# Performance work log

Hardware: AMD Instinct MI355X
Metric: run time of the kernel (lower is better)

The kernel has to match this reference:

```python
import jax, jax.numpy as jnp
import numpy as np

D_MODEL = 1024
D_STATE = 16
D_CONV = 4
EXPAND = 2
HEADDIM = 8
D_INNER = EXPAND * D_MODEL            # 2048
NHEADS = D_INNER // HEADDIM           # 256
CONV_DIM = D_INNER + 2 * D_STATE      # 2080 (ngroups=1)
D_IN_PROJ = 2 * D_INNER + 2 * D_STATE + NHEADS  # 4384
B_SZ, SEQ = 4, 2048
EPS = 1e-5


def setup_inputs() -> dict:
    key = jax.random.key(0)
    ks = jax.random.split(key, 8)
    return {
        "x": jax.random.normal(ks[0], (B_SZ, SEQ, D_MODEL), jnp.float32),
        "ln_w": jnp.ones((D_MODEL,), jnp.float32),
        "ln_b": jnp.zeros((D_MODEL,), jnp.float32),
        "W_in": jax.random.normal(ks[1], (D_MODEL, D_IN_PROJ), jnp.float32) * 0.02,
        "conv_w": jax.random.normal(ks[2], (D_CONV, 1, CONV_DIM), jnp.float32) * 0.2,
        "conv_b": jnp.zeros((CONV_DIM,), jnp.float32),
        "A_log": jnp.log(jax.random.uniform(ks[3], (NHEADS,), jnp.float32, 1.0, 16.0)),
        "Dp": jnp.ones((NHEADS,), jnp.float32) + 0.1 * jax.random.normal(ks[4], (NHEADS,), jnp.float32),
        "dt_bias": 0.5 * jax.random.normal(ks[5], (NHEADS,), jnp.float32),
        "rms_w": jnp.ones((D_INNER,), jnp.float32),
        "W_out": jax.random.normal(ks[6], (D_INNER, D_MODEL), jnp.float32) * 0.02,
    }


def _mamba_block(x, ln_w, ln_b, W_in, conv_w, conv_b, A_log, Dp, dt_bias, rms_w, W_out):
    B, L, _ = x.shape
    # pre-norm LayerNorm
    mu = jnp.mean(x, axis=-1, keepdims=True)
    var = jnp.mean((x - mu) ** 2, axis=-1, keepdims=True)
    xn = (x - mu) * jax.lax.rsqrt(var + EPS) * ln_w + ln_b

    # in_proj -> z, xBC, dt
    u = xn @ W_in                                    # (B, L, 4384)
    z = u[..., :D_INNER]
    xBC = u[..., D_INNER:D_INNER + CONV_DIM]
    dt = jax.nn.softplus(u[..., -NHEADS:] + dt_bias)  # (B, L, NHEADS)

    # causal depthwise conv1d + SiLU
    xp = jnp.pad(xBC, ((0, 0), (D_CONV - 1, 0), (0, 0)))
    xBC = jax.lax.conv_general_dilated(
        xp, conv_w, window_strides=(1,), padding="VALID",
        dimension_numbers=("NWC", "WIO", "NWC"), feature_group_count=CONV_DIM)
    xBC = jax.nn.silu(xBC + conv_b)

    xs = xBC[..., :D_INNER].reshape(B, L, NHEADS, HEADDIM)   # SSM input
    Bm = xBC[..., D_INNER:D_INNER + D_STATE]                  # (B, L, N)
    Cm = xBC[..., D_INNER + D_STATE:]                          # (B, L, N)

    A = -jnp.exp(A_log)                                       # (NHEADS,)

    def step(h, inp):
        # h: (B, H, P, N)
        x_t, B_t, C_t, dt_t = inp
        dA = jnp.exp(dt_t * A)                                 # (B, H)
        h = h * dA[..., None, None] + jnp.einsum("bh,bhp,bn->bhpn", dt_t, x_t, B_t)
        y = jnp.einsum("bhpn,bn->bhp", h, C_t)
        return h, y

    h0 = jnp.zeros((B, NHEADS, HEADDIM, D_STATE), x.dtype)
    _, ys = jax.lax.scan(step, h0, (xs.swapaxes(0, 1), Bm.swapaxes(0, 1),
                                     Cm.swapaxes(0, 1), dt.swapaxes(0, 1)))
    y = ys.swapaxes(0, 1) + Dp[None, None, :, None] * xs       # (B, L, H, P)
    y = y.reshape(B, L, D_INNER)

    # gated RMSNorm: rmsnorm(y * silu(z)) * weight
    g = y * jax.nn.silu(z)
    g = g * jax.lax.rsqrt(jnp.mean(g * g, axis=-1, keepdims=True) + EPS) * rms_w

    return x + g @ W_out


def reference(x, ln_w, ln_b, W_in, conv_w, conv_b, A_log, Dp, dt_bias, rms_w, W_out):
    return _mamba_block(x, ln_w, ln_b, W_in, conv_w, conv_b, A_log, Dp, dt_bias, rms_w, W_out)
```

## Files before the change

kernel.cpp:

```cpp
#include <hip/hip_runtime.h>

typedef __bf16 bf16;
typedef __attribute__((ext_vector_type(8))) __bf16 bf16x8;
typedef __attribute__((ext_vector_type(4))) float f32x4;

#define B_SZ 4
#define SEQ 2048
#define DM 1024
#define DIN 2048
#define NH 256
#define DSTATE 16
#define CONVD 2080
#define DPROJ 4384
#define NPAD1 4608
#define MROWS 8192
#define NC 64
#define LC 32
#define UROWB 8768

__device__ __forceinline__ void gload_lds16(const void* g, void* l) {
  __builtin_amdgcn_global_load_lds(
      (__attribute__((address_space(1))) void*)g,
      (__attribute__((address_space(3))) void*)l, 16, 0, 0);
}

template <int N>
__device__ __forceinline__ void vm_wait() {
  asm volatile("s_waitcnt vmcnt(%0)" ::"n"(N) : "memory");
}
__device__ __forceinline__ void bar() { asm volatile("s_barrier" ::: "memory"); }

__global__ void transpose_cvt(const float* __restrict__ W, bf16* __restrict__ WT,
                              int K, int N, int Npad) {
  __shared__ float tile[32][33];
  int k0 = blockIdx.x * 32, n0 = blockIdx.y * 32;
  int tx = threadIdx.x, ty = threadIdx.y;
#pragma unroll
  for (int j = 0; j < 4; j++) {
    int k = k0 + ty + 8 * j, n = n0 + tx;
    tile[ty + 8 * j][tx] = (k < K && n < N) ? W[(size_t)k * N + n] : 0.f;
  }
  __syncthreads();
#pragma unroll
  for (int j = 0; j < 4; j++) {
    int n = n0 + ty + 8 * j, k = k0 + tx;
    if (n < Npad && k < K) WT[(size_t)n * K + k] = (bf16)tile[tx][ty + 8 * j];
  }
}

__global__ __launch_bounds__(256) void ln_kernel(const float* __restrict__ x,
                                                 const float* __restrict__ lw,
                                                 const float* __restrict__ lb,
                                                 bf16* __restrict__ xn) {
  int row = blockIdx.x;
  int t = threadIdx.x;
  f32x4 v4 = ((const f32x4*)(x + (size_t)row * DM))[t];
  float v0 = v4[0], v1 = v4[1], v2 = v4[2], v3 = v4[3];
  float s = v0 + v1 + v2 + v3;
  float s2 = v0 * v0 + v1 * v1 + v2 * v2 + v3 * v3;
#pragma unroll
  for (int off = 32; off > 0; off >>= 1) {
    s += __shfl_down(s, off);
    s2 += __shfl_down(s2, off);
  }
  __shared__ float ps[8];
  int wave = t >> 6, lane = t & 63;
  if (lane == 0) { ps[wave] = s; ps[4 + wave] = s2; }
  __syncthreads();
  s = ps[0] + ps[1] + ps[2] + ps[3];
  s2 = ps[4] + ps[5] + ps[6] + ps[7];
  float mean = s * (1.f / DM);
  float var = s2 * (1.f / DM) - mean * mean;
  float rstd = rsqrtf(var + 1e-5f);
  f32x4 wv = ((const f32x4*)lw)[t];
  f32x4 bv = ((const f32x4*)lb)[t];
  bf16 o[4];
  o[0] = (bf16)((v0 - mean) * rstd * wv[0] + bv[0]);
  o[1] = (bf16)((v1 - mean) * rstd * wv[1] + bv[1]);
  o[2] = (bf16)((v2 - mean) * rstd * wv[2] + bv[2]);
  o[3] = (bf16)((v3 - mean) * rstd * wv[3] + bv[3]);
  bf16* dst = xn + (size_t)row * DM + t * 4;
  dst[0] = o[0]; dst[1] = o[1]; dst[2] = o[2]; dst[3] = o[3];
}

#define PHASE(MQ, NQ, P, STAGE_STMT)                                                       \
  {                                                                                        \
    const char* sa_ = lds + ((P) * 2 + MQ) * 16384;                                        \
    const char* sb_ = lds + 65536 + ((P) * 2 + NQ) * 16384;                                \
    bf16x8 a_[4][2], b_[2][2];                                                             \
    _Pragma("unroll") for (int mi = 0; mi < 4; mi++) {                                     \
      int lrow = wm * 64 + mi * 16 + lr16;                                                 \
      a_[mi][0] = *(const bf16x8*)(sa_ + lrow * 128 + ts0 * 16);                           \
      a_[mi][1] = *(const bf16x8*)(sa_ + lrow * 128 + ts1 * 16);                           \
    }                                                                                      \
    _Pragma("unroll") for (int ni = 0; ni < 2; ni++) {                                     \
      int lrow = wn * 32 + ni * 16 + lr16;                                                 \
      b_[ni][0] = *(const bf16x8*)(sb_ + lrow * 128 + ts0 * 16);                           \
      b_[ni][1] = *(const bf16x8*)(sb_ + lrow * 128 + ts1 * 16);                           \
    }                                                                                      \
    STAGE_STMT;                                                                            \
    __builtin_amdgcn_s_setprio(1);                                                         \
    _Pragma("unroll") for (int mi = 0; mi < 4; mi++)                                       \
      _Pragma("unroll") for (int ni = 0; ni < 2; ni++) {                                   \
        acc[MQ * 4 + mi][NQ * 2 + ni] = __builtin_amdgcn_mfma_f32_16x16x32_bf16(           \
            a_[mi][0], b_[ni][0], acc[MQ * 4 + mi][NQ * 2 + ni], 0, 0, 0);                 \
        acc[MQ * 4 + mi][NQ * 2 + ni] = __builtin_amdgcn_mfma_f32_16x16x32_bf16(           \
            a_[mi][1], b_[ni][1], acc[MQ * 4 + mi][NQ * 2 + ni], 0, 0, 0);                 \
      }                                                                                    \
    __builtin_amdgcn_s_setprio(0);                                                         \
  }

__global__ __launch_bounds__(512, 2) void gemm1_8p(const bf16* __restrict__ A,
                                                   const bf16* __restrict__ BT,
                                                   bf16* __restrict__ C) {
  __shared__ char lds[131072];
  int bid = blockIdx.x;
  int swz = (bid & 7) * 72 + (bid >> 3);
  int bm = swz / 18, bn = swz - (swz / 18) * 18;
  int m0 = bm * 256, n0 = bn * 256;
  int t = threadIdx.x, lane = t & 63, wave = t >> 6;
  int wm = wave >> 2, wn = wave & 3;
  int lr16 = lane & 15, kq = lane >> 4;
  int ts0 = kq ^ (lr16 & 7);
  int ts1 = (4 + kq) ^ (lr16 & 7);
  int sw = (lane & 7) ^ ((lane >> 3) & 7);
  int l8 = lane >> 3;
  int c0 = 2 * wave, c1 = 2 * wave + 1;
  int lr0 = c0 * 8 + l8, lr1 = c1 * 8 + l8;
  const char* Ab = (const char*)A;
  const char* Bb = (const char*)BT;
  int grA0 = m0 + (lr0 >> 6) * 128 + (lr0 & 63);
  int grA1 = m0 + (lr1 >> 6) * 128 + (lr1 & 63);
  int gcB0 = n0 + (lr0 >> 5) * 64 + (lr0 & 31);
  int gcB1 = n0 + (lr1 >> 5) * 64 + (lr1 & 31);

  auto stA = [&](int kt, int p, int mq) {
    char* slot = lds + (p * 2 + mq) * 16384;
    size_t ko = (size_t)kt * 128 + sw * 16;
    gload_lds16(Ab + (size_t)(grA0 + mq * 64) * 2048 + ko, slot + c0 * 1024);
    gload_lds16(Ab + (size_t)(grA1 + mq * 64) * 2048 + ko, slot + c1 * 1024);
  };
  auto stB = [&](int kt, int p, int nq) {
    char* slot = lds + 65536 + (p * 2 + nq) * 16384;
    size_t ko = (size_t)kt * 128 + sw * 16;
    gload_lds16(Bb + (size_t)(gcB0 + nq * 32) * 2048 + ko, slot + c0 * 1024);
    gload_lds16(Bb + (size_t)(gcB1 + nq * 32) * 2048 + ko, slot + c1 * 1024);
  };

  f32x4 acc[8][4] = {};
  stA(0, 0, 0); stB(0, 0, 0); stA(0, 0, 1); stB(0, 0, 1); stA(1, 1, 0); stB(1, 1, 0);
#pragma unroll 1
  for (int kt = 0; kt < 16; kt++) {
    int p = kt & 1;
    if (kt < 15) vm_wait<8>(); else vm_wait<4>();
    bar();
    PHASE(0, 0, p, { if (kt + 1 < 16) stA(kt + 1, p ^ 1, 1); });
    if (kt < 15) vm_wait<6>(); else vm_wait<0>();
    bar();
    PHASE(0, 1, p, { if (kt + 1 < 16) stB(kt + 1, p ^ 1, 1); });
    bar();
    PHASE(1, 0, p, { if (kt + 2 < 16) stA(kt + 2, p, 0); });
    bar();
    PHASE(1, 1, p, { if (kt + 2 < 16) stB(kt + 2, p, 0); });
  }
#pragma unroll
  for (int mq = 0; mq < 2; mq++)
#pragma unroll
    for (int mi = 0; mi < 4; mi++)
#pragma unroll
      for (int nq = 0; nq < 2; nq++)
#pragma unroll
        for (int ni = 0; ni < 2; ni++) {
          int row = m0 + wm * 128 + mq * 64 + mi * 16 + kq * 4;
          int col = n0 + wn * 64 + nq * 32 + ni * 16 + lr16;
          f32x4 v = acc[mq * 4 + mi][nq * 2 + ni];
          if (col < 4384) {
#pragma unroll
            for (int r = 0; r < 4; r++)
              C[(size_t)(row + r) * DPROJ + col] = (bf16)v[r];
          }
        }
}

__global__ __launch_bounds__(256) void gemm2_kernel(const bf16* __restrict__ A,
                                                    const bf16* __restrict__ BT,
                                                    int K, int ldc,
                                                    float* __restrict__ C,
                                                    const float* __restrict__ Xres) {
  __shared__ bf16 As[128 * 32];
  __shared__ bf16 Bs[128 * 32];
  int m0 = blockIdx.y * 128, n0 = blockIdx.x * 128;
  int t = threadIdx.x;
  int lane = t & 63, wave = t >> 6;
  int wm = wave >> 1, wn = wave & 1;
  int lr = lane & 15, kq = lane >> 4;
  f32x4 acc[4][4] = {};
  const char* Ab = (const char*)A;
  const char* Bb = (const char*)BT;
  size_t strideA = (size_t)K * 2;
  int r0 = t >> 2;
  int kb0 = (t & 3) * 16;
  int nk = K / 32;
  for (int kt = 0; kt < nk; ++kt) {
    size_t koff = (size_t)kt * 64;
    gload_lds16(Ab + (size_t)(m0 + r0) * strideA + koff + kb0, (char*)As + wave * 1024);
    gload_lds16(Ab + (size_t)(m0 + 64 + r0) * strideA + koff + kb0, (char*)As + 4096 + wave * 1024);
    gload_lds16(Bb + (size_t)(n0 + r0) * strideA + koff + kb0, (char*)Bs + wave * 1024);
    gload_lds16(Bb + (size_t)(n0 + 64 + r0) * strideA + koff + kb0, (char*)Bs + 4096 + wave * 1024);
    __syncthreads();
    bf16x8 af[4], bfr[4];
#pragma unroll
    for (int i = 0; i < 4; i++) af[i] = *(const bf16x8*)&As[(wm * 64 + i * 16 + lr) * 32 + kq * 8];
#pragma unroll
    for (int j = 0; j < 4; j++) bfr[j] = *(const bf16x8*)&Bs[(wn * 64 + j * 16 + lr) * 32 + kq * 8];
#pragma unroll
    for (int i = 0; i < 4; i++)
#pragma unroll
      for (int j = 0; j < 4; j++)
        acc[i][j] = __builtin_amdgcn_mfma_f32_16x16x32_bf16(af[i], bfr[j], acc[i][j], 0, 0, 0);
    __syncthreads();
  }
#pragma unroll
  for (int i = 0; i < 4; i++) {
    int row = m0 + wm * 64 + i * 16 + kq * 4;
#pragma unroll
    for (int j = 0; j < 4; j++) {
      int col = n0 + wn * 64 + j * 16 + lr;
#pragma unroll
      for (int r = 0; r < 4; r++) {
        size_t o = (size_t)(row + r) * ldc + col;
        C[o] = Xres[o] + acc[i][j][r];
      }
    }
  }
}

__global__ __launch_bounds__(256) void conv_prep3(const bf16* __restrict__ u,
                                                  const float* __restrict__ cw,
                                                  const float* __restrict__ cb,
                                                  const float* __restrict__ dt_bias,
                                                  bf16* __restrict__ xs,
                                                  float* __restrict__ BC,
                                                  float* __restrict__ dtf) {
  const int JPR = 292;
  int idx = blockIdx.x * 256 + threadIdx.x;
  if (idx >= MROWS * JPR) return;
  int row = idx / JPR;
  int j = idx - row * JPR;
  int t = row & (SEQ - 1);
  if (j < 260) {
    int c0 = j * 8;
    float acc[8];
#pragma unroll
    for (int i = 0; i < 8; i++) acc[i] = cb[c0 + i];
    const bf16* ub = u + (size_t)row * DPROJ + DIN + c0;
#pragma unroll
    for (int tap = 0; tap < 4; tap++) {
      int tt = t - 3 + tap;
      if (tt >= 0) {
        bf16x8 uv = *(const bf16x8*)(ub + (ptrdiff_t)(tap - 3) * DPROJ);
        const float* wv = cw + tap * CONVD + c0;
#pragma unroll
        for (int i = 0; i < 8; i++) acc[i] += wv[i] * (float)uv[i];
      }
    }
    if (c0 < DIN) {
      bf16x8 o;
#pragma unroll
      for (int i = 0; i < 8; i++) {
        float sv = acc[i] / (1.f + __expf(-acc[i]));
        o[i] = (bf16)sv;
      }
      *(bf16x8*)(xs + (size_t)row * DIN + c0) = o;
    } else {
      float* bc = BC + (size_t)row * 32 + (c0 - DIN);
#pragma unroll
      for (int i = 0; i < 8; i++) bc[i] = acc[i] / (1.f + __expf(-acc[i]));
    }
  } else {
    int h0 = (j - 260) * 8;
    bf16x8 uv = *(const bf16x8*)(u + (size_t)row * DPROJ + (DPROJ - NH) + h0);
    float* dst = dtf + (size_t)row * NH + h0;
#pragma unroll
    for (int i = 0; i < 8; i++) {
      float xv = (float)uv[i] + dt_bias[h0 + i];
      dst[i] = (xv > 20.f) ? xv : log1pf(__expf(xv));
    }
  }
}

__global__ __launch_bounds__(64) void scan_p1(const bf16* __restrict__ xs,
                                              const float* __restrict__ BC,
                                              const float* __restrict__ dtf,
                                              const float* __restrict__ A_log,
                                              bf16* __restrict__ uscr) {
  int c = blockIdx.x & 63, hg = (blockIdx.x >> 6) & 31, b = blockIdx.x >> 11;
  int lane = threadIdx.x, hh = lane >> 3;
  int h = hg * 8 + hh;
  float A = -__expf(A_log[h]);
  float st[16];
#pragma unroll
  for (int n = 0; n < 16; n++) st[n] = 0.f;
  float pcum = 1.f;
  size_t rb = (size_t)b * SEQ + (size_t)c * LC;
  for (int t = 0; t < LC; t++) {
    size_t row = rb + t;
    const float* bcrow = BC + row * 32;
    float dtv = dtf[row * NH + h];
    float x = (float)xs[row * DIN + hg * 64 + lane];
    float dA = __expf(dtv * A);
    pcum *= dA;
    float w = dtv * x;
#pragma unroll
    for (int n = 0; n < 16; n++) st[n] = st[n] * dA + w * bcrow[n];
  }
  char* slot = (char*)uscr + (size_t)blockIdx.x * UROWB + 4096;
  float* S = (float*)slot;
#pragma unroll
  for (int n = 0; n < 16; n++) S[lane * 16 + n] = st[n];
  if ((lane & 7) == 0) ((float*)(slot + 4096))[hh] = pcum;
}

__global__ __launch_bounds__(64) void scan_p2(bf16* __restrict__ uscr) {
  int bh = blockIdx.x;
  int lane = threadIdx.x, hh = lane >> 3;
  float H[16];
#pragma unroll
  for (int n = 0; n < 16; n++) H[n] = 0.f;
  char* base = (char*)uscr + (size_t)bh * NC * UROWB + 4096;
  float sN[16], PN;
  {
    float* S = (float*)base;
#pragma unroll
    for (int n = 0; n < 16; n++) sN[n] = S[lane * 16 + n];
    PN = ((const float*)(base + 4096))[hh];
  }
  for (int c = 0; c < NC; c++) {
    float sC[16], PC = PN;
#pragma unroll
    for (int n = 0; n < 16; n++) sC[n] = sN[n];
    if (c + 1 < NC) {
      char* slot = base + (size_t)(c + 1) * UROWB;
      float* S = (float*)slot;
#pragma unroll
      for (int n = 0; n < 16; n++) sN[n] = S[lane * 16 + n];
      PN = ((const float*)(slot + 4096))[hh];
    }
    float* S0 = (float*)(base + (size_t)c * UROWB);
#pragma unroll
    for (int n = 0; n < 16; n++) {
      float hn = H[n];
      S0[lane * 16 + n] = hn;
      H[n] = PC * hn + sC[n];
    }
  }
}

__global__ __launch_bounds__(64) void scan_p3(const bf16* __restrict__ xs,
                                              const float* __restrict__ BC,
                                              const float* __restrict__ dtf,
                                              const float* __restrict__ A_log,
                                              const float* __restrict__ Dp,
                                              const bf16* __restrict__ uscr,
                                              bf16* __restrict__ y) {
  int c = blockIdx.x & 63, hg = (blockIdx.x >> 6) & 31, b = blockIdx.x >> 11;
  int lane = threadIdx.x, hh = lane >> 3;
  int h = hg * 8 + hh;
  float A = -__expf(A_log[h]);
  float D = Dp[h];
  const char* slot = (const char*)uscr + (size_t)blockIdx.x * UROWB + 4096;
  float st[16];
#pragma unroll
  for (int n = 0; n < 16; n++) st[n] = ((const float*)slot)[lane * 16 + n];
  size_t rb = (size_t)b * SEQ + (size_t)c * LC;
  for (int t = 0; t < LC; t++) {
    size_t row = rb + t;
    const float* bcrow = BC + row * 32;
    float dtv = dtf[row * NH + h];
    float x = (float)xs[row * DIN + hg * 64 + lane];
    float dA = __expf(dtv * A);
    float w = dtv * x;
    float yv = 0.f;
#pragma unroll
    for (int n = 0; n < 16; n++) {
      st[n] = st[n] * dA + w * bcrow[n];
      yv += st[n] * bcrow[16 + n];
    }
    y[row * DIN + hg * 64 + lane] = (bf16)(yv + D * x);
  }
}

__global__ __launch_bounds__(256) void gate_rms(const bf16* __restrict__ u,
                                                const bf16* __restrict__ y,
                                                const float* __restrict__ rms_w,
                                                bf16* __restrict__ g) {
  int row = blockIdx.x;
  int t = threadIdx.x;
  bf16x8 zv = ((const bf16x8*)(u + (size_t)row * DPROJ))[t];
  bf16x8 yv = ((const bf16x8*)(y + (size_t)row * DIN))[t];
  float gv[8];
  float s2 = 0.f;
#pragma unroll
  for (int i = 0; i < 8; i++) {
    float z = (float)zv[i];
    float yy = (float)yv[i];
    float gg = yy * z / (1.f + __expf(-z));
    gv[i] = gg;
    s2 += gg * gg;
  }
#pragma unroll
  for (int off = 32; off > 0; off >>= 1) s2 += __shfl_down(s2, off);
  __shared__ float ps[4];
  int wave = t >> 6, lane = t & 63;
  if (lane == 0) ps[wave] = s2;
  __syncthreads();
  s2 = ps[0] + ps[1] + ps[2] + ps[3];
  float scale = rsqrtf(s2 * (1.f / DIN) + 1e-5f);
  f32x4 w0 = ((const f32x4*)rms_w)[2 * t];
  f32x4 w1 = ((const f32x4*)rms_w)[2 * t + 1];
  bf16x8 og;
#pragma unroll
  for (int i = 0; i < 4; i++) og[i] = (bf16)(gv[i] * scale * w0[i]);
#pragma unroll
  for (int i = 0; i < 4; i++) og[4 + i] = (bf16)(gv[4 + i] * scale * w1[i]);
  ((bf16x8*)(g + (size_t)row * DIN))[t] = og;
}

extern "C" void kernel_launch(void* const* d_in, const int* in_sizes, int n_in,
                              void* d_out, int out_size, void* d_ws, size_t ws_size,
                              hipStream_t stream) {
  const float* x = (const float*)d_in[0];
  const float* lnw = (const float*)d_in[1];
  const float* lnb = (const float*)d_in[2];
  const float* Win = (const float*)d_in[3];
  const float* cw = (const float*)d_in[4];
  const float* cb = (const float*)d_in[5];
  const float* Alog = (const float*)d_in[6];
  const float* Dpv = (const float*)d_in[7];
  const float* dtb = (const float*)d_in[8];
  const float* rmsw = (const float*)d_in[9];
  const float* Wout = (const float*)d_in[10];
  float* out = (float*)d_out;

  char* ws = (char*)d_ws;
  bf16* u = (bf16*)(ws + 0);
  bf16* xnb = (bf16*)(ws + 71827456);
  bf16* WinT = (bf16*)(ws + 88604672);
  bf16* yb = (bf16*)(ws + 71827456);
  bf16* xsb = (bf16*)(ws + 105381888);
  bf16* gb = (bf16*)(ws + 105381888);
  float* BC = (float*)(ws + 138936320);
  float* dtf = (float*)(ws + 139984896);
  bf16* WoutT = (bf16*)(ws + 148373504);

  transpose_cvt<<<dim3(32, 144), dim3(32, 8), 0, stream>>>(Win, WinT, 1024, DPROJ, NPAD1);
  transpose_cvt<<<dim3(64, 32), dim3(32, 8), 0, stream>>>(Wout, WoutT, DIN, DM, DM);
  ln_kernel<<<MROWS, 256, 0, stream>>>(x, lnw, lnb, xnb);
  gemm1_8p<<<576, 512, 0, stream>>>(xnb, WinT, u);
  conv_prep3<<<(MROWS * 292) / 256, 256, 0, stream>>>(u, cw, cb, dtb, xsb, BC, dtf);
  scan_p1<<<MROWS, 64, 0, stream>>>(xsb, BC, dtf, Alog, u);
  scan_p2<<<128, 64, 0, stream>>>(u);
  scan_p3<<<MROWS, 64, 0, stream>>>(xsb, BC, dtf, Alog, Dpv, u, yb);
  gate_rms<<<MROWS, 256, 0, stream>>>(u, yb, rmsw, gb);
  gemm2_kernel<<<dim3(DM / 128, MROWS / 128), 256, 0, stream>>>(gb, WoutT, DIN, DM, out, x);
}
```

Before: 324.4 us.

## Replace simple out-proj GEMM with 8-wave pipelined kernel; restructure gemm1 phase barriers

The simple 128x128 out-projection GEMM, which synchronised twice per K step with no prefetch, is replaced by a 512-thread 256x128-tile kernel. The new kernel uses the same double-buffered, swizzled global-to-LDS staging and phased MFMA scheme as the in-projection GEMM. The in-projection GEMM's phase macro is also reworked: barriers and an explicit LDS-count wait now bracket each MFMA cluster, and the vm waits are moved into the phases. The aim is to overlap loads with compute and cut sync stalls, at the cost of more barriers per iteration and fewer blocks (256) for the second GEMM.

```diff
diff --git a/kernel.cpp b/kernel.cpp
--- a/kernel.cpp
+++ b/kernel.cpp
@@ -29,6 +29,9 @@
   asm volatile("s_waitcnt vmcnt(%0)" ::"n"(N) : "memory");
 }
 __device__ __forceinline__ void bar() { asm volatile("s_barrier" ::: "memory"); }
+__device__ __forceinline__ void lgkm0() {
+  asm volatile("s_waitcnt lgkmcnt(0)" ::: "memory");
+}
 
 __global__ void transpose_cvt(const float* __restrict__ W, bf16* __restrict__ WT,
                               int K, int N, int Npad) {
@@ -83,10 +86,10 @@
   dst[0] = o[0]; dst[1] = o[1]; dst[2] = o[2]; dst[3] = o[3];
 }
 
-#define PHASE(MQ, NQ, P, STAGE_STMT)                                                       \
+#define G1_PHASE(MQ, NQ, P, STAGE, VMW)                                                    \
   {                                                                                        \
-    const char* sa_ = lds + ((P) * 2 + MQ) * 16384;                                        \
-    const char* sb_ = lds + 65536 + ((P) * 2 + NQ) * 16384;                                \
+    const char* sa_ = lds + ((P) * 2 + (MQ)) * 16384;                                      \
+    const char* sb_ = lds + 65536 + ((P) * 2 + (NQ)) * 16384;                              \
     bf16x8 a_[4][2], b_[2][2];                                                             \
     _Pragma("unroll") for (int mi = 0; mi < 4; mi++) {                                     \
       int lrow = wm * 64 + mi * 16 + lr16;                                                 \
@@ -98,16 +101,20 @@
       b_[ni][0] = *(const bf16x8*)(sb_ + lrow * 128 + ts0 * 16);                           \
       b_[ni][1] = *(const bf16x8*)(sb_ + lrow * 128 + ts1 * 16);                           \
     }                                                                                      \
-    STAGE_STMT;                                                                            \
+    STAGE;                                                                                 \
+    VMW;                                                                                   \
+    bar();                                                                                 \
+    lgkm0();                                                                               \
     __builtin_amdgcn_s_setprio(1);                                                         \
     _Pragma("unroll") for (int mi = 0; mi < 4; mi++)                                       \
       _Pragma("unroll") for (int ni = 0; ni < 2; ni++) {                                   \
-        acc[MQ * 4 + mi][NQ * 2 + ni] = __builtin_amdgcn_mfma_f32_16x16x32_bf16(           \
-            a_[mi][0], b_[ni][0], acc[MQ * 4 + mi][NQ * 2 + ni], 0, 0, 0);                 \
-        acc[MQ * 4 + mi][NQ * 2 + ni] = __builtin_amdgcn_mfma_f32_16x16x32_bf16(           \
-            a_[mi][1], b_[ni][1], acc[MQ * 4 + mi][NQ * 2 + ni], 0, 0, 0);                 \
+        acc[(MQ) * 4 + mi][(NQ) * 2 + ni] = __builtin_amdgcn_mfma_f32_16x16x32_bf16(       \
+            a_[mi][0], b_[ni][0], acc[(MQ) * 4 + mi][(NQ) * 2 + ni], 0, 0, 0);             \
+        acc[(MQ) * 4 + mi][(NQ) * 2 + ni] = __builtin_amdgcn_mfma_f32_16x16x32_bf16(       \
+            a_[mi][1], b_[ni][1], acc[(MQ) * 4 + mi][(NQ) * 2 + ni], 0, 0, 0);             \
       }                                                                                    \
     __builtin_amdgcn_s_setprio(0);                                                         \
+    bar();                                                                                 \
   }
 
 __global__ __launch_bounds__(512, 2) void gemm1_8p(const bf16* __restrict__ A,
@@ -149,19 +156,17 @@
 
   f32x4 acc[8][4] = {};
   stA(0, 0, 0); stB(0, 0, 0); stA(0, 0, 1); stB(0, 0, 1); stA(1, 1, 0); stB(1, 1, 0);
+  vm_wait<8>();
+  bar();
 #pragma unroll 1
   for (int kt = 0; kt < 16; kt++) {
     int p = kt & 1;
-    if (kt < 15) vm_wait<8>(); else vm_wait<4>();
-    bar();
-    PHASE(0, 0, p, { if (kt + 1 < 16) stA(kt + 1, p ^ 1, 1); });
-    if (kt < 15) vm_wait<6>(); else vm_wait<0>();
-    bar();
-    PHASE(0, 1, p, { if (kt + 1 < 16) stB(kt + 1, p ^ 1, 1); });
-    bar();
-    PHASE(1, 0, p, { if (kt + 2 < 16) stA(kt + 2, p, 0); });
-    bar();
-    PHASE(1, 1, p, { if (kt + 2 < 16) stB(kt + 2, p, 0); });
+    G1_PHASE(0, 0, p, { if (kt + 1 < 16) stA(kt + 1, p ^ 1, 1); },
+             { if (kt < 15) vm_wait<6>(); else vm_wait<0>(); });
+    G1_PHASE(0, 1, p, { if (kt + 1 < 16) stB(kt + 1, p ^ 1, 1); }, {});
+    G1_PHASE(1, 0, p, { if (kt + 2 < 16) stA(kt + 2, p, 0); }, {});
+    G1_PHASE(1, 1, p, { if (kt + 2 < 16) stB(kt + 2, p, 0); },
+             { if (kt < 14) vm_wait<8>(); else if (kt == 14) vm_wait<4>(); });
   }
 #pragma unroll
   for (int mq = 0; mq < 2; mq++)
@@ -182,57 +187,101 @@
         }
 }
 
-__global__ __launch_bounds__(256) void gemm2_kernel(const bf16* __restrict__ A,
-                                                    const bf16* __restrict__ BT,
-                                                    int K, int ldc,
-                                                    float* __restrict__ C,
-                                                    const float* __restrict__ Xres) {
-  __shared__ bf16 As[128 * 32];
-  __shared__ bf16 Bs[128 * 32];
-  int m0 = blockIdx.y * 128, n0 = blockIdx.x * 128;
-  int t = threadIdx.x;
-  int lane = t & 63, wave = t >> 6;
-  int wm = wave >> 1, wn = wave & 1;
-  int lr = lane & 15, kq = lane >> 4;
-  f32x4 acc[4][4] = {};
+#define G2_PHASE(MQ, P, STAGE, VMW)                                                        \
+  {                                                                                        \
+    const char* sa_ = lds + ((P) * 2 + (MQ)) * 16384;                                      \
+    const char* sb_ = lds + 65536 + (P) * 16384;                                           \
+    bf16x8 a_[4][2], b_[2][2];                                                             \
+    _Pragma("unroll") for (int mi = 0; mi < 4; mi++) {                                     \
+      int lrow = wm * 64 + mi * 16 + lr16;                                                 \
+      a_[mi][0] = *(const bf16x8*)(sa_ + lrow * 128 + ts0 * 16);                           \
+      a_[mi][1] = *(const bf16x8*)(sa_ + lrow * 128 + ts1 * 16);                           \
+    }                                                                                      \
+    _Pragma("unroll") for (int ni = 0; ni < 2; ni++) {                                     \
+      int lrow = wn * 32 + ni * 16 + lr16;                                                 \
+      b_[ni][0] = *(const bf16x8*)(sb_ + lrow * 128 + ts0 * 16);                           \
+      b_[ni][1] = *(const bf16x8*)(sb_ + lrow * 128 + ts1 * 16);                           \
+    }                                                                                      \
+    STAGE;                                                                                 \
+    VMW;                                                                                   \
+    bar();                                                                                 \
+    lgkm0();                                                                               \
+    __builtin_amdgcn_s_setprio(1);                                                         \
+    _Pragma("unroll") for (int mi = 0; mi < 4; mi++)                                       \
+      _Pragma("unroll") for (int ni = 0; ni < 2; ni++) {                                   \
+        acc[(MQ) * 4 + mi][ni] = __builtin_amdgcn_mfma_f32_16x16x32_bf16(                  \
+            a_[mi][0], b_[ni][0], acc[(MQ) * 4 + mi][ni], 0, 0, 0);                        \
+        acc[(MQ) * 4 + mi][ni] = __builtin_amdgcn_mfma_f32_16x16x32_bf16(                  \
+            a_[mi][1], b_[ni][1], acc[(MQ) * 4 + mi][ni], 0, 0, 0);                        \
+      }                                                                                    \
+    __builtin_amdgcn_s_setprio(0);                                                         \
+    bar();                                                                                 \
+  }
+
+__global__ __launch_bounds__(512, 2) void gemm2_8p(const bf16* __restrict__ A,
+                                                   const bf16* __restrict__ BT,
+                                                   float* __restrict__ C,
+                                                   const float* __restrict__ Xres) {
+  __shared__ char lds[98304];
+  int bid = blockIdx.x;
+  int swz = (bid & 7) * 32 + (bid >> 3);
+  int bm = swz >> 3, bn = swz & 7;
+  int m0 = bm * 256, n0 = bn * 128;
+  int t = threadIdx.x, lane = t & 63, wave = t >> 6;
+  int wm = wave >> 2, wn = wave & 3;
+  int lr16 = lane & 15, kq = lane >> 4;
+  int ts0 = kq ^ (lr16 & 7);
+  int ts1 = (4 + kq) ^ (lr16 & 7);
+  int sw = (lane & 7) ^ ((lane >> 3) & 7);
+  int l8 = lane >> 3;
+  int c0 = 2 * wave, c1 = 2 * wave + 1;
+  int lr0 = c0 * 8 + l8, lr1 = c1 * 8 + l8;
   const char* Ab = (const char*)A;
   const char* Bb = (const char*)BT;
-  size_t strideA = (size_t)K * 2;
-  int r0 = t >> 2;
-  int kb0 = (t & 3) * 16;
-  int nk = K / 32;
-  for (int kt = 0; kt < nk; ++kt) {
-    size_t koff = (size_t)kt * 64;
-    gload_lds16(Ab + (size_t)(m0 + r0) * strideA + koff + kb0, (char*)As + wave * 1024);
-    gload_lds16(Ab + (size_t)(m0 + 64 + r0) * strideA + koff + kb0, (char*)As + 4096 + wave * 1024);
-    gload_lds16(Bb + (size_t)(n0 + r0) * strideA + koff + kb0, (char*)Bs + wave * 1024);
-    gload_lds16(Bb + (size_t)(n0 + 64 + r0) * strideA + koff + kb0, (char*)Bs + 4096 + wave * 1024);
-    __syncthreads();
-    bf16x8 af[4], bfr[4];
-#pragma unroll
-    for (int i = 0; i < 4; i++) af[i] = *(const bf16x8*)&As[(wm * 64 + i * 16 + lr) * 32 + kq * 8];
-#pragma unroll
-    for (int j = 0; j < 4; j++) bfr[j] = *(const bf16x8*)&Bs[(wn * 64 + j * 16 + lr) * 32 + kq * 8];
-#pragma unroll
-    for (int i = 0; i < 4; i++)
-#pragma unroll
-      for (int j = 0; j < 4; j++)
-        acc[i][j] = __builtin_amdgcn_mfma_f32_16x16x32_bf16(af[i], bfr[j], acc[i][j], 0, 0, 0);
-    __syncthreads();
-  }
-#pragma unroll
-  for (int i = 0; i < 4; i++) {
-    int row = m0 + wm * 64 + i * 16 + kq * 4;
-#pragma unroll
-    for (int j = 0; j < 4; j++) {
-      int col = n0 + wn * 64 + j * 16 + lr;
-#pragma unroll
-      for (int r = 0; r < 4; r++) {
-        size_t o = (size_t)(row + r) * ldc + col;
-        C[o] = Xres[o] + acc[i][j][r];
+  int grA0 = m0 + (lr0 >> 6) * 128 + (lr0 & 63);
+  int grA1 = m0 + (lr1 >> 6) * 128 + (lr1 & 63);
+  int gcB0 = n0 + lr0, gcB1 = n0 + lr1;
+
+  auto stA = [&](int kt, int p, int mq) {
+    char* slot = lds + (p * 2 + mq) * 16384;
+    size_t ko = (size_t)kt * 128 + sw * 16;
+    gload_lds16(Ab + (size_t)(grA0 + mq * 64) * 4096 + ko, slot + c0 * 1024);
+    gload_lds16(Ab + (size_t)(grA1 + mq * 64) * 4096 + ko, slot + c1 * 1024);
+  };
+  auto stB = [&](int kt, int p) {
+    char* slot = lds + 65536 + p * 16384;
+    size_t ko = (size_t)kt * 128 + sw * 16;
+    gload_lds16(Bb + (size_t)gcB0 * 4096 + ko, slot + c0 * 1024);
+    gload_lds16(Bb + (size_t)gcB1 * 4096 + ko, slot + c1 * 1024);
+  };
+
+  f32x4 acc[8][2] = {};
+  stA(0, 0, 0); stB(0, 0); stA(0, 0, 1); stA(1, 1, 0);
+  vm_wait<4>();
+  bar();
+#pragma unroll 1
+  for (int kt = 0; kt < 32; kt++) {
+    int p = kt & 1;
+    G2_PHASE(0, p, { if (kt + 1 < 32) { stB(kt + 1, p ^ 1); stA(kt + 1, p ^ 1, 1); } },
+             { if (kt < 31) vm_wait<6>(); else vm_wait<0>(); });
+    G2_PHASE(1, p, { if (kt + 2 < 32) stA(kt + 2, p, 0); },
+             { if (kt < 30) vm_wait<4>(); else if (kt == 30) vm_wait<2>(); });
+  }
+#pragma unroll
+  for (int mq = 0; mq < 2; mq++)
+#pragma unroll
+    for (int mi = 0; mi < 4; mi++)
+#pragma unroll
+      for (int ni = 0; ni < 2; ni++) {
+        int row = m0 + wm * 128 + mq * 64 + mi * 16 + kq * 4;
+        int col = n0 + wn * 32 + ni * 16 + lr16;
+        f32x4 v = acc[mq * 4 + mi][ni];
+#pragma unroll
+        for (int r = 0; r < 4; r++) {
+          size_t o = (size_t)(row + r) * DM + col;
+          C[o] = Xres[o] + v[r];
+        }
       }
-    }
-  }
 }
 
 __global__ __launch_bounds__(256) void conv_prep3(const bf16* __restrict__ u,
@@ -462,5 +511,5 @@
   scan_p2<<<128, 64, 0, stream>>>(u);
   scan_p3<<<MROWS, 64, 0, stream>>>(xsb, BC, dtf, Alog, Dpv, u, yb);
   gate_rms<<<MROWS, 256, 0, stream>>>(u, yb, rmsw, gb);
-  gemm2_kernel<<<dim3(DM / 128, MROWS / 128), 256, 0, stream>>>(gb, WoutT, DIN, DM, out, x);
-}
+  gemm2_8p<<<256, 512, 0, stream>>>(gb, WoutT, out, x);
+}
```

New measurement: 321.5 us. No clear change (-0.9%).
